# Kernel tuning notes

Measured on AMD Instinct MI355X. Metric: run time of the kernel, lower is better.

The kernel has to match this reference:

```python
import jax, jax.numpy as jnp
import numpy as np
import math

B, N, D, H, T = 256, 512, 512, 8, 128
HD = D // H
CLIP = 10.0
CAP = 1.0
NEG = -1.0e9


def setup_inputs() -> dict:
    key = jax.random.key(0)
    ks = jax.random.split(key, 12)
    s = 1.0 / math.sqrt(D)
    return {
        "embeddings": jax.random.normal(ks[0], (B, N, D), jnp.float32),
        "mean_graph_emb": jax.random.normal(ks[1], (B, D), jnp.float32),
        "used_capacity": jax.random.uniform(ks[2], (T, B), jnp.float32),
        "Wk": jax.random.normal(ks[3], (D, D), jnp.float32) * s,
        "Wk_tanh": jax.random.normal(ks[4], (D, D), jnp.float32) * s,
        "Wv": jax.random.normal(ks[5], (D, D), jnp.float32) * s,
        "Wq_context": jax.random.normal(ks[6], (D, D), jnp.float32) * s,
        "Wq_step": jax.random.normal(ks[7], (D + 1, D), jnp.float32) * s,
        "Wout": jax.random.normal(ks[8], (D, D), jnp.float32) * s,
        "prev_a": jax.random.randint(ks[9], (T, B), 0, N, jnp.int32),
        "mask": jax.random.randint(ks[10], (T, B, N), 0, 2, jnp.int32),
    }


def reference(embeddings, mean_graph_emb, used_capacity, Wk, Wk_tanh, Wv,
              Wq_context, Wq_step, Wout, prev_a, mask):
    # Projections (done once per graph embedding, as in get_projections)
    K = (embeddings @ Wk).reshape(B, N, H, HD).transpose(0, 2, 1, 3)      # [B,H,N,hd]
    V = (embeddings @ Wv).reshape(B, N, H, HD).transpose(0, 2, 1, 3)      # [B,H,N,hd]
    K_tanh = embeddings @ Wk_tanh                                          # [B,N,D]
    Q_context = mean_graph_emb @ Wq_context                                # [B,D]

    inv_sqrt_hd = 1.0 / math.sqrt(HD)
    inv_sqrt_d = 1.0 / math.sqrt(D)

    def step(carry, xs):
        prev_t, cap_t, mask_t = xs  # [B], [B], [B,N]
        # get_step_context: gather prev node embedding + remaining capacity
        cur_emb = jnp.take_along_axis(embeddings, prev_t[:, None, None], axis=1)[:, 0]  # [B,D]
        step_ctx = jnp.concatenate([cur_emb, (CAP - cap_t)[:, None]], axis=-1)          # [B,D+1]
        q = Q_context + step_ctx @ Wq_step                                               # [B,D]
        qh = q.reshape(B, H, HD)                                                          # [B,H,hd]
        # decoder MHA, seq_len_q = 1
        logits = jnp.einsum("bhd,bhnd->bhn", qh, K) * inv_sqrt_hd                        # [B,H,N]
        logits = jnp.where(mask_t[:, None, :] == 1, NEG, logits)
        attn = jax.nn.softmax(logits, axis=-1)
        mha = jnp.einsum("bhn,bhnd->bhd", attn, V).reshape(B, D) @ Wout                  # [B,D]
        # single-head tanh-clipped pointer logits
        comp = jnp.einsum("bd,bnd->bn", mha, K_tanh) * inv_sqrt_d                        # [B,N]
        comp = jnp.tanh(comp) * CLIP
        comp = jnp.where(mask_t == 1, NEG, comp)
        p = jax.nn.softmax(comp, axis=-1)                                                # [B,N]
        return carry, p

    _, ps = jax.lax.scan(step, None, (prev_a, used_capacity, mask))  # [T,B,N]
    return ps.transpose(1, 0, 2)  # [B,T,N]
```

## Files before the change

kernel.cpp:

```cpp
#include <hip/hip_runtime.h>
#include <hip/hip_bf16.h>

constexpr int Bb = 256;
constexpr int Nn = 512;
constexpr int Dd = 512;
constexpr int Hh = 8;
constexpr int Tt = 128;
#define NEGF (-1.0e9f)

typedef __attribute__((ext_vector_type(4))) float f32x4;
typedef __attribute__((ext_vector_type(8))) short bf16x8;
typedef __attribute__((ext_vector_type(8))) unsigned short u16x8;

#define AS1 __attribute__((address_space(1)))
#define AS3 __attribute__((address_space(3)))

__device__ __forceinline__ unsigned short f2bf(float f) {
  union { float f; unsigned u; } v; v.f = f;
  unsigned r = v.u + 0x7fffu + ((v.u >> 16) & 1u);
  return (unsigned short)(r >> 16);
}

__device__ __forceinline__ unsigned cvtpk(float lo, float hi) {
  unsigned r;
  asm("v_cvt_pk_bf16_f32 %0, %1, %2" : "=v"(r) : "v"(lo), "v"(hi));
  return r;
}

__global__ void cast_emb_k(const float* __restrict__ src, unsigned short* __restrict__ dst, int n8) {
  int i = blockIdx.x * 256 + threadIdx.x;
  if (i >= n8) return;
  const float4* s = (const float4*)src + (size_t)i * 2;
  float4 a = s[0], b = s[1];
  u16x8 o;
  o[0] = f2bf(a.x); o[1] = f2bf(a.y); o[2] = f2bf(a.z); o[3] = f2bf(a.w);
  o[4] = f2bf(b.x); o[5] = f2bf(b.y); o[6] = f2bf(b.z); o[7] = f2bf(b.w);
  ((u16x8*)dst)[i] = o;
}

__global__ void cast_wt_k(const float* __restrict__ W0, const float* __restrict__ W1,
                          const float* __restrict__ W2, const float* __restrict__ W3,
                          unsigned short* __restrict__ D0, unsigned short* __restrict__ D1,
                          unsigned short* __restrict__ D2, unsigned short* __restrict__ D3) {
  int mid = blockIdx.x >> 8;
  int tile = blockIdx.x & 255;
  const float* S = (mid == 0) ? W0 : (mid == 1) ? W1 : (mid == 2) ? W2 : W3;
  unsigned short* Dst = (mid == 0) ? D0 : (mid == 1) ? D1 : (mid == 2) ? D2 : D3;
  __shared__ float t[32][33];
  int r0 = (tile >> 4) * 32, c0 = (tile & 15) * 32;
  int tx = threadIdx.x & 31, ty = threadIdx.x >> 5;
#pragma unroll
  for (int yy = 0; yy < 4; ++yy) {
    int r = ty + yy * 8;
    t[r][tx] = S[(size_t)(r0 + r) * 512 + c0 + tx];
  }
  __syncthreads();
#pragma unroll
  for (int yy = 0; yy < 4; ++yy) {
    int c = ty + yy * 8;
    Dst[(size_t)(c0 + c) * 512 + r0 + tx] = f2bf(t[tx][c]);
  }
}

__global__ void mbits_k(const int* __restrict__ mask, unsigned* __restrict__ bits) {
  size_t gid = (size_t)blockIdx.x * 256 + threadIdx.x;
  int mv = mask[gid];
  unsigned long long bal = __ballot(mv == 1);
  if ((threadIdx.x & 63) == 0) {
    unsigned t = (unsigned)(gid >> 17);
    unsigned b = (unsigned)((gid >> 9) & 255);
    unsigned n = (unsigned)(gid & 511);
    unsigned* dst = bits + (((size_t)b * 128 + t) * 16 + (n >> 5));
    dst[0] = (unsigned)bal;
    dst[1] = (unsigned)(bal >> 32);
  }
}

__device__ __forceinline__ void stage_tile(const unsigned short* __restrict__ G, int row0, int k0,
                                           unsigned short* lds_base, int wave, int lane) {
#pragma unroll
  for (int c = 0; c < 4; ++c) {
    int chunk = wave * 4 + c;
    const unsigned short* g = G + (size_t)(row0 + chunk * 8 + (lane >> 3)) * 512 + k0 + (lane & 7) * 8;
    __builtin_amdgcn_global_load_lds((AS1 void*)g, (AS3 void*)(lds_base + chunk * 512), 16, 0, 0);
  }
}

template <int MODE>
__global__ __launch_bounds__(256, 2)
void gemm5_k(const unsigned short* __restrict__ A, const unsigned short* __restrict__ BT,
             void* __restrict__ Cout,
             const float* __restrict__ Qc, const float* __restrict__ WqsL,
             const float* __restrict__ capp, const int* __restrict__ prev) {
  __shared__ __align__(16) char lds[32768];
  unsigned short* ldsA = (unsigned short*)lds;
  unsigned short* ldsB = ldsA + 8192;
  int xcd = blockIdx.x & 7, loc = blockIdx.x >> 3;
  int ml = loc >> 2, nt = loc & 3;
  int mt = xcd * 32 + ml;
  int m0 = mt * 128, n0 = nt * 128;
  int tid = threadIdx.x, lane = tid & 63, w = tid >> 6;
  int wm = w >> 1, wn = w & 1;
  int l15 = lane & 15, l4 = lane >> 4;

  const unsigned short* gbase[4];
#pragma unroll
  for (int c = 0; c < 4; ++c) {
    int row = m0 + (w * 4 + c) * 8 + (lane >> 3);
    if (MODE == 3) {
      int t = row >> 8, bb = row & 255;
      int pa = prev[t * Bb + bb];
      gbase[c] = A + (size_t)(bb * 512 + pa) * 512 + (lane & 7) * 8;
    } else {
      gbase[c] = A + (size_t)row * 512 + (lane & 7) * 8;
    }
  }

  f32x4 acc[4][4] = {};
  for (int k0 = 0; k0 < 512; k0 += 64) {
#pragma unroll
    for (int c = 0; c < 4; ++c) {
      int chunk = w * 4 + c;
      __builtin_amdgcn_global_load_lds((AS1 void*)(gbase[c] + k0),
                                       (AS3 void*)(ldsA + chunk * 512), 16, 0, 0);
    }
    stage_tile(BT, n0, k0, ldsB, w, lane);
    __syncthreads();
#pragma unroll
    for (int ks = 0; ks < 2; ++ks) {
      bf16x8 fa[4], fb[4];
#pragma unroll
      for (int ii = 0; ii < 4; ++ii)
        fa[ii] = *(const bf16x8*)(ldsA + (wm * 64 + ii * 16 + l15) * 64 + ks * 32 + l4 * 8);
#pragma unroll
      for (int jj = 0; jj < 4; ++jj)
        fb[jj] = *(const bf16x8*)(ldsB + (wn * 64 + jj * 16 + l15) * 64 + ks * 32 + l4 * 8);
#pragma unroll
      for (int ii = 0; ii < 4; ++ii)
#pragma unroll
        for (int jj = 0; jj < 4; ++jj)
          acc[ii][jj] = __builtin_amdgcn_mfma_f32_16x16x32_bf16(fa[ii], fb[jj], acc[ii][jj], 0, 0, 0);
    }
    __syncthreads();
  }

  if (MODE == 1) {
    unsigned short* C = (unsigned short*)Cout;
#pragma unroll
    for (int ii = 0; ii < 4; ++ii)
#pragma unroll
      for (int jj = 0; jj < 4; ++jj)
#pragma unroll
        for (int r = 0; r < 4; ++r) {
          int row = m0 + wm * 64 + ii * 16 + l4 * 4 + r;
          int col = n0 + wn * 64 + jj * 16 + l15;
          C[(size_t)row * 512 + col] = f2bf(acc[ii][jj][r]);
        }
  } else {
    unsigned short* C = (unsigned short*)Cout;
#pragma unroll
    for (int ii = 0; ii < 4; ++ii)
#pragma unroll
      for (int jj = 0; jj < 4; ++jj)
#pragma unroll
        for (int r = 0; r < 4; ++r) {
          int row = m0 + wm * 64 + ii * 16 + l4 * 4 + r;
          int col = n0 + wn * 64 + jj * 16 + l15;
          int t = row >> 8, bbx = row & 255;
          float val = acc[ii][jj][r] + Qc[(size_t)bbx * 512 + col] + (1.0f - capp[row]) * WqsL[col];
          C[(size_t)(bbx * 128 + t) * 512 + col] = f2bf(val * 0.125f);
        }
  }
}

template <int OUTF>
__global__ __launch_bounds__(256, 2)
void smallgemm_k(const unsigned short* __restrict__ A, const unsigned short* __restrict__ BT,
                 void* __restrict__ Cout) {
  __shared__ __align__(16) char lds[32768];
  unsigned short* ldsA = (unsigned short*)lds;
  unsigned short* ldsB = ldsA + 8192;
  int mt = blockIdx.x >> 2, nt = blockIdx.x & 3;
  int m0 = mt * 128, n0 = nt * 128;
  int tid = threadIdx.x, lane = tid & 63, w = tid >> 6;
  int wm = w >> 1, wn = w & 1;
  int l15 = lane & 15, l4 = lane >> 4;

  f32x4 acc[4][4] = {};
  for (int k0 = 0; k0 < 512; k0 += 64) {
    stage_tile(A, m0, k0, ldsA, w, lane);
    stage_tile(BT, n0, k0, ldsB, w, lane);
    __syncthreads();
#pragma unroll
    for (int ks = 0; ks < 2; ++ks) {
      bf16x8 fa[4], fb[4];
#pragma unroll
      for (int ii = 0; ii < 4; ++ii)
        fa[ii] = *(const bf16x8*)(ldsA + (wm * 64 + ii * 16 + l15) * 64 + ks * 32 + l4 * 8);
#pragma unroll
      for (int jj = 0; jj < 4; ++jj)
        fb[jj] = *(const bf16x8*)(ldsB + (wn * 64 + jj * 16 + l15) * 64 + ks * 32 + l4 * 8);
#pragma unroll
      for (int ii = 0; ii < 4; ++ii)
#pragma unroll
        for (int jj = 0; jj < 4; ++jj)
          acc[ii][jj] = __builtin_amdgcn_mfma_f32_16x16x32_bf16(fa[ii], fb[jj], acc[ii][jj], 0, 0, 0);
    }
    __syncthreads();
  }
#pragma unroll
  for (int ii = 0; ii < 4; ++ii)
#pragma unroll
    for (int jj = 0; jj < 4; ++jj)
#pragma unroll
      for (int r = 0; r < 4; ++r) {
        int row = m0 + wm * 64 + ii * 16 + l4 * 4 + r;
        int col = n0 + wn * 64 + jj * 16 + l15;
        if (OUTF) ((float*)Cout)[(size_t)row * 512 + col] = acc[ii][jj][r];
        else ((unsigned short*)Cout)[(size_t)row * 512 + col] = f2bf(acc[ii][jj][r]);
      }
}

#define STAGE10(SLOT, MAT, H, ROWB, KT)                                            \
  do {                                                                             \
    const unsigned short* G_ = (MAT) ? BT : A;                                     \
    int rb_ = (ROWB) + (H) * 128;                                                  \
    char* Lb_ = lds + (SLOT) * 65536 + (MAT) * 32768 + (H) * 16384;                \
    _Pragma("unroll")                                                              \
    for (int sh_ = 0; sh_ < 2; ++sh_) {                                            \
      int off_ = sh_ * 8192 + tid * 16;                                            \
      int r_ = off_ >> 7;                                                          \
      int c_ = (off_ & 127) ^ ((r_ & 7) << 4);     \
      const char* g_ = (const char*)(G_ + (size_t)(rb_ + r_) * 512 + (KT) * 64) + c_; \
      __builtin_amdgcn_global_load_lds((AS1 void*)g_, (AS3 void*)(Lb_ + off_), 16, 0, 0); \
    }                                                                              \
  } while (0)

#define LDA_Q(QM)                                                   \
  _Pragma("unroll")                                                 \
  for (int ii = 0; ii < 4; ++ii) {                                  \
    int rr_ = (QM) * 64 + ii * 16 + l15;                            \
    const char* ap_ = ldsAh + rr_ * 128;                            \
    int sw_ = (rr_ & 7) << 4;                                       \
    fa[ii][0] = *(const bf16x8*)(ap_ + ((l4 * 16) ^ sw_));          \
    fa[ii][1] = *(const bf16x8*)(ap_ + ((64 + l4 * 16) ^ sw_));     \
  }

#define LDB_Q(QN)                                                   \
  _Pragma("unroll")                                                 \
  for (int jj = 0; jj < 2; ++jj) {                                  \
    int rr_ = (wn & 1) * 64 + (QN) * 32 + jj * 16 + l15;            \
    const char* bp_ = ldsBh + rr_ * 128;                            \
    int sw_ = (rr_ & 7) << 4;                                       \
    fb[jj][0] = *(const bf16x8*)(bp_ + ((l4 * 16) ^ sw_));          \
    fb[jj][1] = *(const bf16x8*)(bp_ + ((64 + l4 * 16) ^ sw_));     \
  }

#define MM16(QM, QN)                                                              \
  do {                                                                            \
    __builtin_amdgcn_s_setprio(1);                                                \
    _Pragma("unroll")                                                             \
    for (int ii = 0; ii < 4; ++ii)                                                \
      _Pragma("unroll")                                                           \
      for (int jj = 0; jj < 2; ++jj) {                                            \
        acc[(QM) * 4 + ii][(QN) * 2 + jj] = __builtin_amdgcn_mfma_f32_16x16x32_bf16( \
            fa[ii][0], fb[jj][0], acc[(QM) * 4 + ii][(QN) * 2 + jj], 0, 0, 0);    \
        acc[(QM) * 4 + ii][(QN) * 2 + jj] = __builtin_amdgcn_mfma_f32_16x16x32_bf16( \
            fa[ii][1], fb[jj][1], acc[(QM) * 4 + ii][(QN) * 2 + jj], 0, 0, 0);    \
      }                                                                           \
    __builtin_amdgcn_s_setprio(0);                                                \
  } while (0)

__global__ __launch_bounds__(512, 1)
void gemm10_k(const unsigned short* __restrict__ A,
              const unsigned short* __restrict__ B0, const unsigned short* __restrict__ B1,
              unsigned short* __restrict__ C0, unsigned short* __restrict__ C2) {
  __shared__ __align__(16) char lds[131072];
  int xcd = blockIdx.x & 7, loc = blockIdx.x >> 3;
  int ml4 = loc >> 2, cmb = loc & 3;
  int grp = cmb >> 1, nh = cmb & 1;
  const unsigned short* BT = grp ? B1 : B0;
  int mtb = xcd * 64 + ml4 * 4;
  int n0 = nh * 256;
  int tid = threadIdx.x, lane = tid & 63, w = tid >> 6;
  int wm = w >> 2, wn = w & 3;
  int l15 = lane & 15, l4 = lane >> 4;

  f32x4 acc[8][4] = {};
  bf16x8 fa[4][2], fb[2][2];

  {
    int m0n = mtb * 256;
    STAGE10(0, 0, 0, m0n, 0); STAGE10(0, 0, 1, m0n, 0);
    STAGE10(0, 1, 0, n0, 0);  STAGE10(0, 1, 1, n0, 0);
  }

  for (int g = 0; g < 32; ++g) {
    int s = g & 1, sn = s ^ 1;
    char* ldsAh = lds + s * 65536 + wm * 16384;
    char* ldsBh = lds + s * 65536 + 32768 + (wn >> 1) * 16384;
    int gn = g + 1;
    int m0n = (mtb + (gn >> 3)) * 256;
    int ktn = gn & 7;
    if (g < 31) {
      STAGE10(sn, 0, 0, m0n, ktn);
      asm volatile("s_waitcnt vmcnt(2)" ::: "memory");
    } else {
      asm volatile("s_waitcnt vmcnt(0)" ::: "memory");
    }
    __builtin_amdgcn_s_barrier();
    LDA_Q(0); LDB_Q(0);
    MM16(0, 0);
    __builtin_amdgcn_s_barrier();
    LDB_Q(1);
    if (g < 31) STAGE10(sn, 0, 1, m0n, ktn);
    __builtin_amdgcn_s_barrier();
    MM16(0, 1);
    __builtin_amdgcn_s_barrier();
    LDA_Q(1);
    if (g < 31) STAGE10(sn, 1, 0, n0, ktn);
    __builtin_amdgcn_s_barrier();
    MM16(1, 1);
    __builtin_amdgcn_s_barrier();
    LDB_Q(0);
    if (g < 31) STAGE10(sn, 1, 1, n0, ktn);
    __builtin_amdgcn_s_barrier();
    MM16(1, 0);
    __builtin_amdgcn_s_barrier();

    if ((g & 7) == 7) {
      int m0cur = (mtb + (g >> 3)) * 256;
      if (grp == 0) {
#pragma unroll
        for (int mi = 0; mi < 8; ++mi)
#pragma unroll
          for (int nj = 0; nj < 4; ++nj)
#pragma unroll
            for (int r = 0; r < 4; ++r) {
              int row = m0cur + wm * 128 + mi * 16 + l4 * 4 + r;
              int col = n0 + wn * 64 + nj * 16 + l15;
              C0[(size_t)row * 512 + col] = f2bf(acc[mi][nj][r]);
            }
      } else {
        int bb = m0cur >> 9, nn0 = m0cur & 511;
        char* wb = lds + 65536 + w * 8192;
#pragma unroll
        for (int p = 0; p < 4; ++p) {
#pragma unroll
          for (int mi = 0; mi < 8; ++mi) {
            ushort4 w4;
            w4.x = f2bf(acc[mi][p][0]);
            w4.y = f2bf(acc[mi][p][1]);
            w4.z = f2bf(acc[mi][p][2]);
            w4.w = f2bf(acc[mi][p][3]);
            *(ushort4*)(wb + l15 * 264 + (mi * 16 + l4 * 4) * 2) = w4;
          }
#pragma unroll
          for (int step = 0; step < 4; ++step) {
            int dl = step * 4 + l4;
            union { ushort4 h[2]; u16x8 v; } u;
            u.h[0] = *(const ushort4*)(wb + dl * 264 + l15 * 16);
            u.h[1] = *(const ushort4*)(wb + dl * 264 + l15 * 16 + 8);
            int dglob = n0 + wn * 64 + p * 16 + dl;
            *(u16x8*)(C2 + (size_t)(bb * 512 + dglob) * 512 + nn0 + wm * 128 + l15 * 8) = u.v;
          }
        }
      }
#pragma unroll
      for (int mi = 0; mi < 8; ++mi)
#pragma unroll
        for (int nj = 0; nj < 4; ++nj)
          acc[mi][nj] = (f32x4){0.f, 0.f, 0.f, 0.f};
      __syncthreads();
    }
  }
}

#define STAGEK5(CH, SLOT)                                                          \
  do {                                                                             \
    _Pragma("unroll")                                                              \
    for (int sh_ = 0; sh_ < 2; ++sh_) {                                            \
      int off_ = sh_ * 8192 + tid * 16;                                            \
      int r_ = off_ >> 7;                                                          \
      int c_ = (off_ & 127) ^ ((r_ & 7) << 4);                                     \
      const char* g_ = (const char*)(Kb + (size_t)(b * 512 + (CH) * 128 + r_) * 512 + h * 64) + c_; \
      __builtin_amdgcn_global_load_lds((AS1 void*)g_, (AS3 void*)(lds + (SLOT) * 16384 + off_), 16, 0, 0); \
    }                                                                              \
  } while (0)

#define STAGEV5(CH, SLOT)                                                          \
  do {                                                                             \
    _Pragma("unroll")                                                              \
    for (int sh_ = 0; sh_ < 2; ++sh_) {                                            \
      int off_ = sh_ * 8192 + tid * 16;                                            \
      int r_ = off_ >> 8;                                                          \
      int c_ = (off_ & 255) ^ ((r_ & 7) << 4);                                     \
      const char* g_ = (const char*)(Vt + (size_t)(b * 512 + h * 64 + r_) * 512 + (CH) * 128) + c_; \
      __builtin_amdgcn_global_load_lds((AS1 void*)g_, (AS3 void*)(lds + 32768 + (SLOT) * 16384 + off_), 16, 0, 0); \
    }                                                                              \
  } while (0)

#define CHUNK5(CH)                                                                 \
  do {                                                                             \
    const char* Ks_ = lds + ((CH) & 1) * 16384;                                    \
    const char* Vs_ = lds + 32768 + ((CH) & 1) * 16384;                            \
    f32x4 sck[8];                                                                  \
    _Pragma("unroll")                                                              \
    for (int jj = 0; jj < 8; ++jj) sck[jj] = (f32x4){0.f, 0.f, 0.f, 0.f};          \
    _Pragma("unroll")                                                              \
    for (int jj = 0; jj < 8; ++jj) {                                               \
      int rr_ = jj * 16 + l15;                                                     \
      int sw_ = (rr_ & 7) << 4;                                                    \
      bf16x8 k0_ = *(const bf16x8*)(Ks_ + rr_ * 128 + ((l4 * 16) ^ sw_));          \
      bf16x8 k1_ = *(const bf16x8*)(Ks_ + rr_ * 128 + ((64 + l4 * 16) ^ sw_));     \
      sck[jj] = __builtin_amdgcn_mfma_f32_16x16x32_bf16(k0_, fq[0], sck[jj], 0, 0, 0); \
      sck[jj] = __builtin_amdgcn_mfma_f32_16x16x32_bf16(k1_, fq[1], sck[jj], 0, 0, 0); \
    }                                                                              \
    unsigned mwarr_[4] = {mqs[CH].x, mqs[CH].y, mqs[CH].z, mqs[CH].w};             \
    float cmx_ = -3.0e38f;                                                         \
    _Pragma("unroll")                                                              \
    for (int jj = 0; jj < 8; ++jj) {                                               \
      unsigned nib_ = mwarr_[jj >> 1] >> (((jj & 1) << 4) + (l4 << 2));            \
      _Pragma("unroll")                                                            \
      for (int r = 0; r < 4; ++r)                                                  \
        sck[jj][r] = ((nib_ >> r) & 1) ? NEGF : sck[jj][r];                        \
      float m01_ = fmaxf(sck[jj][0], sck[jj][1]);                                  \
      float m23_ = fmaxf(sck[jj][2], sck[jj][3]);                                  \
      cmx_ = fmaxf(cmx_, fmaxf(m01_, m23_));                                       \
    }                                                                              \
    cmx_ = fmaxf(cmx_, __shfl_xor(cmx_, 16));                                      \
    cmx_ = fmaxf(cmx_, __shfl_xor(cmx_, 32));                                      \
    float mn_ = fmaxf(mx, cmx_);                                                   \
    float al_ = __expf(mx - mn_);                                                  \
    sum *= al_;                                                                    \
    _Pragma("unroll")                                                              \
    for (int dj = 0; dj < 4; ++dj)                                                 \
      _Pragma("unroll")                                                            \
      for (int r = 0; r < 4; ++r) o[dj][r] *= al_;                                 \
    mx = mn_;                                                                      \
    _Pragma("unroll")                                                              \
    for (int jj = 0; jj < 8; ++jj) {                                               \
      _Pragma("unroll")                                                            \
      for (int r = 0; r < 4; ++r) sck[jj][r] = __expf(sck[jj][r] - mx);            \
      sum += (sck[jj][0] + sck[jj][1]) + (sck[jj][2] + sck[jj][3]);                \
    }                                                                              \
    _Pragma("unroll")                                                              \
    for (int g = 0; g < 4; ++g) {                                                  \
      unsigned a0_ = cvtpk(sck[2 * g][0], sck[2 * g][1]);                          \
      unsigned a1_ = cvtpk(sck[2 * g][2], sck[2 * g][3]);                          \
      unsigned b0_ = cvtpk(sck[2 * g + 1][0], sck[2 * g + 1][1]);                  \
      unsigned b1_ = cvtpk(sck[2 * g + 1][2], sck[2 * g + 1][3]);                  \
      unsigned wA0_ = __shfl(a0_, src0, 64), wB0_ = __shfl(b0_, src0, 64);         \
      unsigned wA1_ = __shfl(a1_, src0, 64), wB1_ = __shfl(b1_, src0, 64);         \
      unsigned wA2_ = __shfl(a0_, src2, 64), wB2_ = __shfl(b0_, src2, 64);         \
      unsigned wA3_ = __shfl(a1_, src2, 64), wB3_ = __shfl(b1_, src2, 64);         \
      union { unsigned u[4]; bf16x8 v; } pu_;                                      \
      pu_.u[0] = loh ? wA0_ : wB0_;                                                \
      pu_.u[1] = loh ? wA1_ : wB1_;                                                \
      pu_.u[2] = loh ? wA2_ : wB2_;                                                \
      pu_.u[3] = loh ? wA3_ : wB3_;                                                \
      _Pragma("unroll")                                                            \
      for (int dj = 0; dj < 4; ++dj) {                                             \
        int rr_ = dj * 16 + l15;                                                   \
        int sw_ = (rr_ & 7) << 4;                                                  \
        bf16x8 fv_ = *(const bf16x8*)(Vs_ + rr_ * 256 + ((g * 64 + l4 * 16) ^ sw_)); \
        o[dj] = __builtin_amdgcn_mfma_f32_16x16x32_bf16(fv_, pu_.v, o[dj], 0, 0, 0); \
      }                                                                            \
    }                                                                              \
  } while (0)

__global__ __launch_bounds__(512, 4)
void attn5_k(const unsigned short* __restrict__ Qb, const unsigned short* __restrict__ Kb,
             const unsigned short* __restrict__ Vt, const unsigned* __restrict__ mbits,
             unsigned short* __restrict__ mhaB) {
  __shared__ __align__(16) char lds[65536];
  int bid = blockIdx.x;
  int h = bid & 7, b = bid >> 3;
  int tid = threadIdx.x, lane = tid & 63, w = tid >> 6;
  int l15 = lane & 15, l4 = lane >> 4;
  int t = w * 16 + l15;

  bf16x8 fq[2];
#pragma unroll
  for (int ks = 0; ks < 2; ++ks)
    fq[ks] = *(const bf16x8*)(Qb + (size_t)(b * 128 + t) * 512 + h * 64 + ks * 32 + l4 * 8);
  uint4 mqs[4];
  {
    const uint4* mp = (const uint4*)(mbits + (((size_t)b * 128 + t) << 4));
    mqs[0] = mp[0]; mqs[1] = mp[1]; mqs[2] = mp[2]; mqs[3] = mp[3];
  }

  float mx = -3.0e38f, sum = 0.f;
  f32x4 o[4] = {};
  int src0 = l15 + ((l4 & 1) ? 32 : 0);
  int src2 = l15 + ((l4 & 1) ? 48 : 16);
  bool loh = (l4 < 2);

  STAGEK5(0, 0); STAGEV5(0, 0);
  STAGEK5(1, 1); STAGEV5(1, 1);
  asm volatile("s_waitcnt vmcnt(4)" ::: "memory");
  __builtin_amdgcn_s_barrier();
  CHUNK5(0);
  __builtin_amdgcn_s_barrier();
  STAGEK5(2, 0); STAGEV5(2, 0);
  asm volatile("s_waitcnt vmcnt(4)" ::: "memory");
  __builtin_amdgcn_s_barrier();
  CHUNK5(1);
  __builtin_amdgcn_s_barrier();
  STAGEK5(3, 1); STAGEV5(3, 1);
  asm volatile("s_waitcnt vmcnt(4)" ::: "memory");
  __builtin_amdgcn_s_barrier();
  CHUNK5(2);
  __builtin_amdgcn_s_barrier();
  asm volatile("s_waitcnt vmcnt(0)" ::: "memory");
  __builtin_amdgcn_s_barrier();
  CHUNK5(3);

  sum += __shfl_xor(sum, 16);
  sum += __shfl_xor(sum, 32);
  float inv = 1.0f / sum;
#pragma unroll
  for (int dj = 0; dj < 4; ++dj) {
    ushort4 w4;
    w4.x = f2bf(o[dj][0] * inv);
    w4.y = f2bf(o[dj][1] * inv);
    w4.z = f2bf(o[dj][2] * inv);
    w4.w = f2bf(o[dj][3] * inv);
    *(ushort4*)(mhaB + (size_t)(b * 128 + t) * 512 + h * 64 + dj * 16 + l4 * 4) = w4;
  }
}

#define STAGEC5(CH, SLOT)                                                          \
  do {                                                                             \
    _Pragma("unroll")                                                              \
    for (int ps_ = 0; ps_ < 4; ++ps_) {                                            \
      int off_ = ps_ * 8192 + tid * 16;                                            \
      int r_ = off_ >> 10;                                                         \
      int c_ = (off_ & 1023) ^ ((r_ & 7) << 4);                                    \
      const char* g_ = (const char*)(embB + (size_t)(b * 512 + nh * 256 + (CH) * 32 + r_) * 512) + c_; \
      __builtin_amdgcn_global_load_lds((AS1 void*)g_, (AS3 void*)(lds + (SLOT) * 32768 + off_), 16, 0, 0); \
    }                                                                              \
  } while (0)

#define CCHUNK5(CH)                                                                \
  do {                                                                             \
    const char* Es_ = lds + ((CH) & 1) * 32768;                                    \
    _Pragma("unroll")                                                              \
    for (int jjl_ = 0; jjl_ < 2; ++jjl_) {                                         \
      f32x4 sck = (f32x4){0.f, 0.f, 0.f, 0.f};                                     \
      int rr_ = jjl_ * 16 + l15;                                                   \
      const char* ep_ = Es_ + rr_ * 1024;                                          \
      int sw_ = (rr_ & 7) << 4;                                                    \
      _Pragma("unroll")                                                            \
      for (int ks_ = 0; ks_ < 16; ++ks_) {                                         \
        bf16x8 fa_ = *(const bf16x8*)(ep_ + ((ks_ * 64 + l4 * 16) ^ sw_));         \
        sck = __builtin_amdgcn_mfma_f32_16x16x32_bf16(fa_, fb[ks_], sck, 0, 0, 0); \
      }                                                                            \
      unsigned nib_ = mwh[CH] >> ((jjl_ << 4) + (l4 << 2));                        \
      float4 o4_;                                                                  \
      float* po_ = (float*)&o4_;                                                   \
      _Pragma("unroll")                                                            \
      for (int r = 0; r < 4; ++r) {                                                \
        float y_ = sck[r] * 0.044194173824159216f;                                 \
        y_ = fminf(fmaxf(y_, -15.f), 15.f);                                        \
        float e2_ = __expf(2.f * y_);                                              \
        float th_ = (e2_ - 1.f) / (e2_ + 1.f);                                     \
        float p_ = __expf(th_ * 10.f - 10.f);                                      \
        p_ = ((nib_ >> r) & 1) ? 0.f : p_;                                         \
        po_[r] = p_;                                                               \
        sum += p_;                                                                 \
      }                                                                            \
      *(float4*)(out + (size_t)(b * 128 + t) * 512 + nh * 256 + (CH) * 32 + jjl_ * 16 + l4 * 4) = o4_; \
    }                                                                              \
  } while (0)

__global__ __launch_bounds__(512, 2)
void comp5_k(const unsigned short* __restrict__ mh2, const unsigned short* __restrict__ embB,
             const unsigned* __restrict__ mbits, float* __restrict__ out,
             float* __restrict__ sums) {
  __shared__ __align__(16) char lds[65536];
  int b = blockIdx.x >> 1, nh = blockIdx.x & 1;
  int tid = threadIdx.x, lane = tid & 63, w = tid >> 6;
  int l15 = lane & 15, l4 = lane >> 4;
  int t = w * 16 + l15;

  bf16x8 fb[16];
#pragma unroll
  for (int ks = 0; ks < 16; ++ks)
    fb[ks] = *(const bf16x8*)(mh2 + (size_t)(b * 128 + t) * 512 + ks * 32 + l4 * 8);
  unsigned mwh[8];
  {
    const uint4* mp = (const uint4*)(mbits + (((size_t)b * 128 + t) << 4)) + nh * 2;
    uint4 a0 = mp[0], a1 = mp[1];
    mwh[0] = a0.x; mwh[1] = a0.y; mwh[2] = a0.z; mwh[3] = a0.w;
    mwh[4] = a1.x; mwh[5] = a1.y; mwh[6] = a1.z; mwh[7] = a1.w;
  }

  float sum = 0.f;
  STAGEC5(0, 0);
  STAGEC5(1, 1);
  asm volatile("s_waitcnt vmcnt(4)" ::: "memory");
  __builtin_amdgcn_s_barrier();
  CCHUNK5(0);
  __builtin_amdgcn_s_barrier();
  STAGEC5(2, 0);
  asm volatile("s_waitcnt vmcnt(4)" ::: "memory");
  __builtin_amdgcn_s_barrier();
  CCHUNK5(1);
  __builtin_amdgcn_s_barrier();
  STAGEC5(3, 1);
  asm volatile("s_waitcnt vmcnt(4)" ::: "memory");
  __builtin_amdgcn_s_barrier();
  CCHUNK5(2);
  __builtin_amdgcn_s_barrier();
  STAGEC5(4, 0);
  asm volatile("s_waitcnt vmcnt(4)" ::: "memory");
  __builtin_amdgcn_s_barrier();
  CCHUNK5(3);
  __builtin_amdgcn_s_barrier();
  STAGEC5(5, 1);
  asm volatile("s_waitcnt vmcnt(4)" ::: "memory");
  __builtin_amdgcn_s_barrier();
  CCHUNK5(4);
  __builtin_amdgcn_s_barrier();
  STAGEC5(6, 0);
  asm volatile("s_waitcnt vmcnt(4)" ::: "memory");
  __builtin_amdgcn_s_barrier();
  CCHUNK5(5);
  __builtin_amdgcn_s_barrier();
  STAGEC5(7, 1);
  asm volatile("s_waitcnt vmcnt(4)" ::: "memory");
  __builtin_amdgcn_s_barrier();
  CCHUNK5(6);
  __builtin_amdgcn_s_barrier();
  asm volatile("s_waitcnt vmcnt(0)" ::: "memory");
  __builtin_amdgcn_s_barrier();
  CCHUNK5(7);

  sum += __shfl_xor(sum, 16);
  sum += __shfl_xor(sum, 32);
  if (l4 == 0) sums[nh * 32768 + b * 128 + t] = sum;
}

__global__ void norm_k(float* __restrict__ out, const float* __restrict__ sums) {
  int row = blockIdx.x * 4 + (threadIdx.x >> 6);
  int lane = threadIdx.x & 63;
  float inv = 1.0f / (sums[row] + sums[32768 + row]);
  float4* p = (float4*)(out + (size_t)row * 512) + lane;
  float4 a = p[0], b = p[64];
  a.x *= inv; a.y *= inv; a.z *= inv; a.w *= inv;
  b.x *= inv; b.y *= inv; b.z *= inv; b.w *= inv;
  p[0] = a; p[64] = b;
}

extern "C" void kernel_launch(void* const* d_in, const int* in_sizes, int n_in,
                              void* d_out, int out_size, void* d_ws, size_t ws_size,
                              hipStream_t stream) {
  (void)in_sizes; (void)n_in; (void)out_size; (void)ws_size;
  const float* emb  = (const float*)d_in[0];
  const float* mge  = (const float*)d_in[1];
  const float* cap  = (const float*)d_in[2];
  const float* Wk   = (const float*)d_in[3];
  const float* Wkt  = (const float*)d_in[4];
  const float* Wv   = (const float*)d_in[5];
  const float* Wqc  = (const float*)d_in[6];
  const float* Wqs  = (const float*)d_in[7];
  const float* Wout = (const float*)d_in[8];
  const int* prev   = (const int*)d_in[9];
  const int* mask   = (const int*)d_in[10];
  float* out = (float*)d_out;

  char* p = (char*)d_ws;
  auto take = [&](size_t n) { char* q = p; p += (n + 255) & ~(size_t)255; return q; };
  unsigned short* embB = (unsigned short*)take((size_t)131072 * 512 * 2);
  unsigned short* Kb   = (unsigned short*)take((size_t)131072 * 512 * 2);
  unsigned short* Vt   = (unsigned short*)take((size_t)131072 * 512 * 2);
  unsigned short* Qb   = (unsigned short*)take((size_t)32768 * 512 * 2);
  unsigned short* mhaB = (unsigned short*)take((size_t)32768 * 512 * 2);
  unsigned short* mh2  = (unsigned short*)take((size_t)32768 * 512 * 2);
  float*          Qc   = (float*)take((size_t)256 * 512 * 4);
  unsigned*       mbit = (unsigned*)take((size_t)256 * 128 * 16 * 4);
  float*          sums = (float*)take((size_t)2 * 32768 * 4);
  unsigned short* WkT  = (unsigned short*)take(524288);
  unsigned short* WvT  = (unsigned short*)take(524288);
  unsigned short* WqsT = (unsigned short*)take(524288);
  unsigned short* WqcT = (unsigned short*)take(524288);
  unsigned short* WktB = (unsigned short*)take(524288);
  unsigned short* WoutB= (unsigned short*)take(524288);
  unsigned short* WFT  = (unsigned short*)take(524288);
  unsigned short* mgeB = (unsigned short*)take((size_t)256 * 512 * 2);

  cast_emb_k<<<32768, 256, 0, stream>>>(emb, embB, 8388608);
  cast_emb_k<<<128, 256, 0, stream>>>(Wkt, WktB, 32768);
  cast_emb_k<<<128, 256, 0, stream>>>(Wout, WoutB, 32768);
  cast_emb_k<<<64, 256, 0, stream>>>(mge, mgeB, 16384);
  cast_wt_k<<<1024, 256, 0, stream>>>(Wk, Wv, Wqs, Wqc, WkT, WvT, WqsT, WqcT);
  mbits_k<<<65536, 256, 0, stream>>>(mask, mbit);
  wf_cast:
  smallgemm_k<0><<<16, 256, 0, stream>>>(WktB, WoutB, WFT);
  smallgemm_k<1><<<8, 256, 0, stream>>>(mgeB, WqcT, Qc);
  gemm5_k<3><<<1024, 256, 0, stream>>>(embB, WqsT, Qb, Qc, Wqs + 512 * 512, cap, prev);
  gemm10_k<<<512, 512, 0, stream>>>(embB, WkT, WvT, Kb, Vt);
  attn5_k<<<2048, 512, 0, stream>>>(Qb, Kb, Vt, mbit, mhaB);
  gemm5_k<1><<<1024, 256, 0, stream>>>(mhaB, WFT, mh2, nullptr, nullptr, nullptr, nullptr);
  comp5_k<<<512, 512, 0, stream>>>(mh2, embB, mbit, out, sums);
  norm_k<<<8192, 256, 0, stream>>>(out, sums);
}
```

Measured before the change: 534.8 us.

## Triple-buffer A tiles in gemm10 and rework transposed V epilogue staging

The K/V projection GEMM moves from a shared double buffer to a three-slot ring for the A (embedding) tiles, prefetched two k-steps ahead, while the B (weight) tiles keep a separate double buffer. LDS grows from 128 KiB to 160 KiB. The transposed V store epilogue now stages 8-row slices in the current A slot with padded rows and writes full 16-byte vectors. The aim is to hide global-load latency for A and make the transpose writes more efficient, at the cost of more LDS, extra lgkmcnt waits, and a new, subtler buffer-reuse ordering.

```diff
diff --git a/kernel.cpp b/kernel.cpp
--- a/kernel.cpp
+++ b/kernel.cpp
@@ -221,17 +221,30 @@
       }
 }
 
-#define STAGE10(SLOT, MAT, H, ROWB, KT)                                            \
+#define STAGE10A(SLOT, H, ROWB, KT)                                               \
   do {                                                                             \
-    const unsigned short* G_ = (MAT) ? BT : A;                                     \
     int rb_ = (ROWB) + (H) * 128;                                                  \
-    char* Lb_ = lds + (SLOT) * 65536 + (MAT) * 32768 + (H) * 16384;                \
+    char* Lb_ = lds + (SLOT) * 32768 + (H) * 16384;                                \
     _Pragma("unroll")                                                              \
     for (int sh_ = 0; sh_ < 2; ++sh_) {                                            \
       int off_ = sh_ * 8192 + tid * 16;                                            \
       int r_ = off_ >> 7;                                                          \
-      int c_ = (off_ & 127) ^ ((r_ & 7) << 4);     \
-      const char* g_ = (const char*)(G_ + (size_t)(rb_ + r_) * 512 + (KT) * 64) + c_; \
+      int c_ = (off_ & 127) ^ ((r_ & 7) << 4);                                     \
+      const char* g_ = (const char*)(A + (size_t)(rb_ + r_) * 512 + (KT) * 64) + c_; \
+      __builtin_amdgcn_global_load_lds((AS1 void*)g_, (AS3 void*)(Lb_ + off_), 16, 0, 0); \
+    }                                                                              \
+  } while (0)
+
+#define STAGE10B(SLOT, H, KT)                                                      \
+  do {                                                                             \
+    int rb_ = n0 + (H) * 128;                                                      \
+    char* Lb_ = lds + 98304 + (SLOT) * 32768 + (H) * 16384;                        \
+    _Pragma("unroll")                                                              \
+    for (int sh_ = 0; sh_ < 2; ++sh_) {                                            \
+      int off_ = sh_ * 8192 + tid * 16;                                            \
+      int r_ = off_ >> 7;                                                          \
+      int c_ = (off_ & 127) ^ ((r_ & 7) << 4);                                     \
+      const char* g_ = (const char*)(BT + (size_t)(rb_ + r_) * 512 + (KT) * 64) + c_; \
       __builtin_amdgcn_global_load_lds((AS1 void*)g_, (AS3 void*)(Lb_ + off_), 16, 0, 0); \
     }                                                                              \
   } while (0)
@@ -275,7 +288,7 @@
 void gemm10_k(const unsigned short* __restrict__ A,
               const unsigned short* __restrict__ B0, const unsigned short* __restrict__ B1,
               unsigned short* __restrict__ C0, unsigned short* __restrict__ C2) {
-  __shared__ __align__(16) char lds[131072];
+  __shared__ __align__(16) char lds[163840];
   int xcd = blockIdx.x & 7, loc = blockIdx.x >> 3;
   int ml4 = loc >> 2, cmb = loc & 3;
   int grp = cmb >> 1, nh = cmb & 1;
@@ -290,20 +303,22 @@
   bf16x8 fa[4][2], fb[2][2];
 
   {
-    int m0n = mtb * 256;
-    STAGE10(0, 0, 0, m0n, 0); STAGE10(0, 0, 1, m0n, 0);
-    STAGE10(0, 1, 0, n0, 0);  STAGE10(0, 1, 1, n0, 0);
+    int m00 = mtb * 256;
+    STAGE10A(0, 0, m00, 0); STAGE10A(0, 1, m00, 0);
+    STAGE10A(1, 0, m00, 1); STAGE10A(1, 1, m00, 1);
+    STAGE10B(0, 0, 0);      STAGE10B(0, 1, 0);
   }
 
   for (int g = 0; g < 32; ++g) {
-    int s = g & 1, sn = s ^ 1;
-    char* ldsAh = lds + s * 65536 + wm * 16384;
-    char* ldsBh = lds + s * 65536 + 32768 + (wn >> 1) * 16384;
-    int gn = g + 1;
-    int m0n = (mtb + (gn >> 3)) * 256;
-    int ktn = gn & 7;
-    if (g < 31) {
-      STAGE10(sn, 0, 0, m0n, ktn);
+    int As = g % 3, Astg = (g + 2) % 3;
+    int Bs = g & 1, Bstg = Bs ^ 1;
+    char* ldsAh = lds + As * 32768 + wm * 16384;
+    char* ldsBh = lds + 98304 + Bs * 32768 + (wn >> 1) * 16384;
+    int g2 = g + 2;
+    int m0A = (mtb + (g2 >> 3)) * 256, ktA = g2 & 7;
+    int ktB = (g + 1) & 7;
+    if (g < 30) {
+      STAGE10A(Astg, 0, m0A, ktA);
       asm volatile("s_waitcnt vmcnt(2)" ::: "memory");
     } else {
       asm volatile("s_waitcnt vmcnt(0)" ::: "memory");
@@ -313,17 +328,17 @@
     MM16(0, 0);
     __builtin_amdgcn_s_barrier();
     LDB_Q(1);
-    if (g < 31) STAGE10(sn, 0, 1, m0n, ktn);
+    if (g < 30) STAGE10A(Astg, 1, m0A, ktA);
     __builtin_amdgcn_s_barrier();
     MM16(0, 1);
     __builtin_amdgcn_s_barrier();
     LDA_Q(1);
-    if (g < 31) STAGE10(sn, 1, 0, n0, ktn);
+    if (g < 31) STAGE10B(Bstg, 0, ktB);
     __builtin_amdgcn_s_barrier();
     MM16(1, 1);
     __builtin_amdgcn_s_barrier();
     LDB_Q(0);
-    if (g < 31) STAGE10(sn, 1, 1, n0, ktn);
+    if (g < 31) STAGE10B(Bstg, 1, ktB);
     __builtin_amdgcn_s_barrier();
     MM16(1, 0);
     __builtin_amdgcn_s_barrier();
@@ -343,27 +358,31 @@
             }
       } else {
         int bb = m0cur >> 9, nn0 = m0cur & 511;
-        char* wb = lds + 65536 + w * 8192;
-#pragma unroll
-        for (int p = 0; p < 4; ++p) {
-#pragma unroll
-          for (int mi = 0; mi < 8; ++mi) {
-            ushort4 w4;
-            w4.x = f2bf(acc[mi][p][0]);
-            w4.y = f2bf(acc[mi][p][1]);
-            w4.z = f2bf(acc[mi][p][2]);
-            w4.w = f2bf(acc[mi][p][3]);
-            *(ushort4*)(wb + l15 * 264 + (mi * 16 + l4 * 4) * 2) = w4;
+        char* wb = lds + As * 32768 + w * 4096;
+        int rdrow = lane >> 3, nseg = lane & 7;
+#pragma unroll
+        for (int p = 0; p < 8; ++p) {
+          int nj = p >> 1;
+          if ((l15 >> 3) == (p & 1)) {
+            int rowL = l15 & 7;
+#pragma unroll
+            for (int mi = 0; mi < 8; ++mi) {
+              ushort4 w4;
+              w4.x = f2bf(acc[mi][nj][0]);
+              w4.y = f2bf(acc[mi][nj][1]);
+              w4.z = f2bf(acc[mi][nj][2]);
+              w4.w = f2bf(acc[mi][nj][3]);
+              *(ushort4*)(wb + rowL * 272 + (mi * 16 + l4 * 4) * 2) = w4;
+            }
           }
-#pragma unroll
-          for (int step = 0; step < 4; ++step) {
-            int dl = step * 4 + l4;
-            union { ushort4 h[2]; u16x8 v; } u;
-            u.h[0] = *(const ushort4*)(wb + dl * 264 + l15 * 16);
-            u.h[1] = *(const ushort4*)(wb + dl * 264 + l15 * 16 + 8);
-            int dglob = n0 + wn * 64 + p * 16 + dl;
-            *(u16x8*)(C2 + (size_t)(bb * 512 + dglob) * 512 + nn0 + wm * 128 + l15 * 8) = u.v;
-          }
+          asm volatile("s_waitcnt lgkmcnt(0)" ::: "memory");
+          u16x8 v0 = *(const u16x8*)(wb + rdrow * 272 + nseg * 16);
+          u16x8 v1 = *(const u16x8*)(wb + rdrow * 272 + 128 + nseg * 16);
+          int dglob = n0 + wn * 64 + p * 8 + rdrow;
+          unsigned short* dp = C2 + (size_t)(bb * 512 + dglob) * 512 + nn0 + wm * 128;
+          *(u16x8*)(dp + nseg * 8) = v0;
+          *(u16x8*)(dp + 64 + nseg * 8) = v1;
+          asm volatile("s_waitcnt lgkmcnt(0)" ::: "memory");
         }
       }
 #pragma unroll
@@ -696,7 +715,6 @@
   cast_emb_k<<<64, 256, 0, stream>>>(mge, mgeB, 16384);
   cast_wt_k<<<1024, 256, 0, stream>>>(Wk, Wv, Wqs, Wqc, WkT, WvT, WqsT, WqcT);
   mbits_k<<<65536, 256, 0, stream>>>(mask, mbit);
-  wf_cast:
   smallgemm_k<0><<<16, 256, 0, stream>>>(WktB, WoutB, WFT);
   smallgemm_k<1><<<8, 256, 0, stream>>>(mgeB, WqcT, Qc);
   gemm5_k<3><<<1024, 256, 0, stream>>>(embB, WqsT, Qb, Qc, Wqs + 512 * 512, cap, prev);
```

After: 529.0 us. Within noise of the previous version (-1.1%).
